# Optimization experiments

Measured on AMD Instinct MI355X. Metric: run time of the kernel, lower is better.

The kernel has to match this reference:

```python
import jax, jax.numpy as jnp
import numpy as np
from jax import lax

KH, KW = 9, 9
FC_DIM = 1024
C_RED = FC_DIM // 8  # 128
EPS = 1e-5


def conv_bn_relu(x, w, gamma, beta):
    # 3x3 conv, stride 1, pad 1 (NCHW / OIHW), then batch-stat BN + ReLU
    y = lax.conv_general_dilated(x, w, (1, 1), ((1, 1), (1, 1)),
                                 dimension_numbers=('NCHW', 'OIHW', 'NCHW'))
    mean = y.mean(axis=(0, 2, 3))
    var = y.var(axis=(0, 2, 3))
    y = (y - mean[None, :, None, None]) * lax.rsqrt(var + EPS)[None, :, None, None]
    y = y * gamma[None, :, None, None] + beta[None, :, None, None]
    return jnp.maximum(y, 0.0)


def local_weighting(feat, atten, kH, kW):
    # feat: [B,C,H,W]; atten: [B,H,W,kH*kW]
    # out[b,c,h,w] = sum_k atten[b,h,w,k] * feat_padded[b,c,h+dh_k,w+dw_k]
    B, C, H, W = feat.shape
    ph, pw = kH // 2, kW // 2
    fp = jnp.pad(feat, ((0, 0), (0, 0), (ph, ph), (pw, pw)))
    out = jnp.zeros_like(feat)
    k = 0
    for dh in range(kH):
        for dw in range(kW):
            out = out + fp[:, :, dh:dh + H, dw:dw + W] * atten[:, None, :, :, k]
            k += 1
    return out


def setup_inputs() -> dict:
    key = jax.random.key(0)
    ks = jax.random.split(key, 12)
    B, H, W = 4, 64, 64
    sc1 = 1.0 / np.sqrt(FC_DIM * 9)
    sc5 = 1.0 / np.sqrt(C_RED * 9)
    return {
        'low_key': jax.random.normal(ks[0], (B, FC_DIM, H, W), jnp.float32),
        'low_nonkey': jax.random.normal(ks[1], (B, FC_DIM, H, W), jnp.float32),
        'local_atten': jax.random.uniform(ks[2], (B, H, W, KH * KW), jnp.float32),
        'w1': jax.random.normal(ks[3], (C_RED, FC_DIM, 3, 3), jnp.float32) * sc1,
        'g1': jnp.ones((C_RED,), jnp.float32),
        'b1': jnp.zeros((C_RED,), jnp.float32),
        'w4': jax.random.normal(ks[4], (C_RED, FC_DIM, 3, 3), jnp.float32) * sc1,
        'g4': jnp.ones((C_RED,), jnp.float32),
        'b4': jnp.zeros((C_RED,), jnp.float32),
        'w5': jax.random.normal(ks[5], (C_RED, C_RED, 3, 3), jnp.float32) * sc5,
        'g5': jnp.ones((C_RED,), jnp.float32),
        'b5': jnp.zeros((C_RED,), jnp.float32),
        'fc1_w': jax.random.normal(ks[6], (10, C_RED), jnp.float32) * (1.0 / np.sqrt(C_RED)),
        'fc1_b': jnp.zeros((10,), jnp.float32),
        'fc2_w': jax.random.normal(ks[7], (1, 10), jnp.float32) * (1.0 / np.sqrt(10.0)),
        'fc2_b': jnp.zeros((1,), jnp.float32),
    }


def reference(low_key, low_nonkey, local_atten,
              w1, g1, b1, w4, g4, b4, w5, g5, b5,
              fc1_w, fc1_b, fc2_w, fc2_b):
    lk = conv_bn_relu(low_key, w1, g1, b1)          # [B,128,H,W]
    trans = local_weighting(lk, local_atten, KH, KW)
    lnk = conv_bn_relu(low_nonkey, w4, g4, b4)
    out = trans - lnk
    out = conv_bn_relu(out, w5, g5, b5)
    out = out.mean(axis=(2, 3))                      # adaptive avg pool to 1x1 -> [B,128]
    out = out @ fc1_w.T + fc1_b
    out = out @ fc2_w.T + fc2_b                      # [B,1]
    return out
```

## Files before the change

### kernel.cpp

```cpp
#include <hip/hip_runtime.h>
#include <hip/hip_bf16.h>


#define B_ 4
#define CM_ 128

typedef __attribute__((ext_vector_type(8))) short short8;
typedef __attribute__((ext_vector_type(4))) float floatx4;
typedef __attribute__((address_space(3))) unsigned lds_as;
typedef __attribute__((address_space(1))) const unsigned glb_as;

__device__ inline short f2bf(float f) {
  union { float f; unsigned u; } v; v.f = f;
  unsigned r = v.u + 0x7fff + ((v.u >> 16) & 1);
  return (short)(r >> 16);
}

__global__ void wprep_kernel(const float* __restrict__ w, short* __restrict__ wpk,
                             int cin) {
  int e = blockIdx.x * 256 + threadIdx.x;
  if (e >= cin * 9 * 128) return;
  int icb = e & 31;
  int oc = (e >> 5) & 127;
  int tap = (e >> 12) % 9;
  int kb = e / (32 * 128 * 9);
  wpk[e] = f2bf(w[((size_t)oc * cin + kb * 32 + icb) * 9 + tap]);
}

template <int KB>
__global__ void xprep_kernel(const float* __restrict__ x, short* __restrict__ xt) {
  int kb = blockIdx.x >> 4, rg = blockIdx.x & 15;
  int b = blockIdx.y;
  int row = rg * 4 + (threadIdx.x >> 6);
  int col = threadIdx.x & 63;
  const float* xs = x + (((size_t)b * (KB * 32) + kb * 32) * 64 + row) * 64 + col;
  short* xd = xt + ((((size_t)b * KB + kb) * 64 + row) * 64 + col) * 32;
  int sw = (col >> 1) & 3;
#pragma unroll
  for (int u = 0; u < 4; u++) {
    short8 pk;
#pragma unroll
    for (int j = 0; j < 8; j++) pk[j] = f2bf(xs[(size_t)(u * 8 + j) * 4096]);
    *(short8*)(xd + (u ^ sw) * 8) = pk;
  }
}

template <int KB>
__global__ __launch_bounds__(512, 2)
void convm_kernel(const short* __restrict__ xt, const short* __restrict__ wpk,
                  float* __restrict__ y) {
  __shared__ __attribute__((aligned(16))) short lx[16896];
  int tid = threadIdx.x;
  int lane = tid & 63;
  int wv = tid >> 6;
  int n16 = lane & 15, quad = lane >> 4;
  int pb = blockIdx.x;
  int b = pb >> 5, h0 = (pb & 31) * 2;
  int oc0 = blockIdx.y * 64 + (wv & 3) * 16;
  int ng = wv >> 2;

  if (tid < 256) {
    int reg = tid >> 4, dw = tid & 15;
    int bu = reg >> 3, rr = (reg >> 1) & 3, cl = reg & 1;
    *(int*)(lx + bu * 8448 + rr * 2112 + (cl ? 65 : 0) * 32 + dw * 2) = 0;
  }
  if (h0 == 0)
    for (int i = tid; i < 2112; i += 512) {
      int bu = i >= 1056; int o = i - bu * 1056;
      *((int*)lx + bu * 4224 + o) = 0;
    }
  if (h0 == 62)
    for (int i = tid; i < 2112; i += 512) {
      int bu = i >= 1056; int o = i - bu * 1056;
      *((int*)lx + bu * 4224 + 3 * 1056 + o) = 0;
    }

  auto dma = [&](int kb, int buf) {
#pragma unroll
    for (int t = 0; t < 2; t++) {
      int idx = wv * 2 + t;
      int r = idx >> 2, cc = idx & 3;
      int row = h0 - 1 + r;
      if (row >= 0 && row < 64) {
        const short* src = xt + ((((size_t)b * KB + kb) * 64 + row) * 64 + cc * 16) * 32 + lane * 8;
        short* dst = lx + buf * 8448 + r * 2112 + (1 + cc * 16) * 32 + lane * 8;
        __builtin_amdgcn_global_load_lds((glb_as*)src, (lds_as*)dst, 16, 0, 0);
      }
    }
  };

  const short* wb = wpk + (size_t)(oc0 + n16) * 32 + quad * 8;
  short8 afr[9], afn[9];
  dma(0, 0);
#pragma unroll
  for (int t = 0; t < 9; t++) afr[t] = *(const short8*)(wb + t * 4096);

  floatx4 acc[4];
#pragma unroll
  for (int nt = 0; nt < 4; nt++) acc[nt] = (floatx4){0.f, 0.f, 0.f, 0.f};

  for (int kb = 0; kb < KB; kb++) {
    __syncthreads();
    if (kb + 1 < KB) {
      dma(kb + 1, (kb + 1) & 1);
      const short* wn = wb + (size_t)(kb + 1) * 36864;
#pragma unroll
      for (int t = 0; t < 9; t++) afn[t] = *(const short8*)(wn + t * 4096);
    }
    const short* lb = lx + (kb & 1) * 8448;
#pragma unroll
    for (int tap = 0; tap < 9; tap++) {
      int r = tap / 3, s = tap % 3;
      const short* lr = lb + (ng + r) * 2112;
#pragma unroll
      for (int nt = 0; nt < 4; nt++) {
        int c = nt * 16 + n16 + s - 1;
        int uu = quad ^ ((c >> 1) & 3);
        short8 bf = *(const short8*)(lr + (c + 1) * 32 + uu * 8);
        acc[nt] = __builtin_amdgcn_mfma_f32_16x16x32_bf16(afr[tap], bf, acc[nt], 0, 0, 0);
      }
    }
    if (kb + 1 < KB) {
#pragma unroll
      for (int t = 0; t < 9; t++) afr[t] = afn[t];
    }
  }

  int row = h0 + ng, col = lane & 15;
#pragma unroll
  for (int nt = 0; nt < 4; nt++)
#pragma unroll
    for (int rg = 0; rg < 4; rg++) {
      int oc = oc0 + quad * 4 + rg;
      y[(((size_t)b * CM_ + oc) * 64 + row) * 64 + nt * 16 + col] = acc[nt][rg];
    }
}

__global__ void bnstats_kernel(const float* __restrict__ y, const float* __restrict__ g,
                               const float* __restrict__ bt, float2* __restrict__ scsh) {
  int c = blockIdx.x;
  int tid = threadIdx.x;
  float s = 0.f, s2 = 0.f;
  for (int b = 0; b < B_; b++) {
    const float4* p = (const float4*)(y + ((size_t)(b * CM_) + c) * 4096);
    for (int i = tid; i < 1024; i += 256) {
      float4 v = p[i];
      s += v.x + v.y + v.z + v.w;
      s2 += v.x * v.x + v.y * v.y + v.z * v.z + v.w * v.w;
    }
  }
  for (int off = 32; off > 0; off >>= 1) {
    s += __shfl_down(s, off);
    s2 += __shfl_down(s2, off);
  }
  __shared__ float rs[4], rq[4];
  if ((tid & 63) == 0) { rs[tid >> 6] = s; rq[tid >> 6] = s2; }
  __syncthreads();
  if (tid == 0) {
    float S = rs[0] + rs[1] + rs[2] + rs[3];
    float Q = rq[0] + rq[1] + rq[2] + rq[3];
    float mean = S * (1.f / 16384.f);
    float var = Q * (1.f / 16384.f) - mean * mean;
    float sc = g[c] * rsqrtf(var + 1e-5f);
    scsh[c] = make_float2(sc, bt[c] - mean * sc);
  }
}

__global__ __launch_bounds__(256, 2)
void localw_kernel(const float* __restrict__ y1, const float2* __restrict__ scsh1,
                   const float* __restrict__ y4, const float2* __restrict__ scsh4,
                   const float* __restrict__ atten, short* __restrict__ xt5) {
  __shared__ float at[81][65];
  __shared__ float lk[16][9][72];
  int bh = blockIdx.x;
  int b = bh >> 6, h = bh & 63;
  int c0 = blockIdx.y * 16;
  int tid = threadIdx.x;

  const float* ap = atten + ((size_t)b * 4096 + h * 64) * 81;
  for (int e = tid; e < 64 * 81; e += 256) {
    int w_ = e / 81, k = e % 81;
    at[k][w_] = ap[w_ * 81 + k];
  }
  for (int e = tid; e < 16 * 9 * 72; e += 256) {
    int c = e / (9 * 72);
    int rem = e % (9 * 72);
    int r = rem / 72;
    int j = rem % 72;
    int row = h + r - 4;
    int col = j - 4;
    float v = 0.f;
    if (row >= 0 && row < 64 && col >= 0 && col < 64) {
      float2 ss = scsh1[c0 + c];
      v = fmaxf(0.f, y1[((size_t)(b * CM_) + c0 + c) * 4096 + row * 64 + col] * ss.x + ss.y);
    }
    lk[c][r][j] = v;
  }
  __syncthreads();

  int lane = tid & 63;
  int wv = tid >> 6;
  float acc[4] = {0.f, 0.f, 0.f, 0.f};
  for (int r = 0; r < 9; r++) {
    float a[9];
#pragma unroll
    for (int dw = 0; dw < 9; dw++) a[dw] = at[r * 9 + dw][lane];
#pragma unroll
    for (int cc = 0; cc < 4; cc++) {
      int c = wv * 4 + cc;
#pragma unroll
      for (int dw = 0; dw < 9; dw++)
        acc[cc] = fmaf(a[dw], lk[c][r][lane + dw], acc[cc]);
    }
  }
#pragma unroll
  for (int cc = 0; cc < 4; cc++) {
    int c = c0 + wv * 4 + cc;
    float2 ss4 = scsh4[c];
    float lnk = fmaxf(0.f, y4[((size_t)(b * CM_) + c) * 4096 + h * 64 + lane] * ss4.x + ss4.y);
    float dv = acc[cc] - lnk;
    int icb = c & 31;
    int uu = (icb >> 3) ^ ((lane >> 1) & 3);
    xt5[((((size_t)b * 4 + (c >> 5)) * 64 + h) * 64 + lane) * 32 + uu * 8 + (icb & 7)] = f2bf(dv);
  }
}

__global__ void pool_kernel(const float* __restrict__ y, const float2* __restrict__ scsh,
                            float* __restrict__ pooled) {
  int bc = blockIdx.x;
  int c = bc & 127;
  float2 ss = scsh[c];
  const float4* p = (const float4*)(y + (size_t)bc * 4096);
  float s = 0.f;
  for (int i = threadIdx.x; i < 1024; i += 256) {
    float4 v = p[i];
    s += fmaxf(0.f, v.x * ss.x + ss.y) + fmaxf(0.f, v.y * ss.x + ss.y) +
         fmaxf(0.f, v.z * ss.x + ss.y) + fmaxf(0.f, v.w * ss.x + ss.y);
  }
  for (int off = 32; off > 0; off >>= 1) s += __shfl_down(s, off);
  __shared__ float rs[4];
  if ((threadIdx.x & 63) == 0) rs[threadIdx.x >> 6] = s;
  __syncthreads();
  if (threadIdx.x == 0) pooled[bc] = (rs[0] + rs[1] + rs[2] + rs[3]) * (1.f / 4096.f);
}

__global__ void fc_kernel(const float* __restrict__ pooled, const float* __restrict__ fc1w,
                          const float* __restrict__ fc1b, const float* __restrict__ fc2w,
                          const float* __restrict__ fc2b, float* __restrict__ out) {
  int lane = threadIdx.x;
  float p[B_][10];
#pragma unroll
  for (int b = 0; b < B_; b++)
#pragma unroll
    for (int j = 0; j < 10; j++) p[b][j] = 0.f;
  for (int c = lane; c < CM_; c += 64) {
#pragma unroll
    for (int b = 0; b < B_; b++) {
      float pv = pooled[b * CM_ + c];
#pragma unroll
      for (int j = 0; j < 10; j++) p[b][j] = fmaf(pv, fc1w[j * CM_ + c], p[b][j]);
    }
  }
  for (int off = 32; off > 0; off >>= 1)
#pragma unroll
    for (int b = 0; b < B_; b++)
#pragma unroll
      for (int j = 0; j < 10; j++) p[b][j] += __shfl_down(p[b][j], off);
  if (lane == 0) {
    for (int b = 0; b < B_; b++) {
      float o = fc2b[0];
      for (int j = 0; j < 10; j++) o += fc2w[j] * (p[b][j] + fc1b[j]);
      out[b] = o;
    }
  }
}

extern "C" void kernel_launch(void* const* d_in, const int* in_sizes, int n_in,
                              void* d_out, int out_size, void* d_ws, size_t ws_size,
                              hipStream_t stream) {
  const float* low_key    = (const float*)d_in[0];
  const float* low_nonkey = (const float*)d_in[1];
  const float* atten      = (const float*)d_in[2];
  const float* w1  = (const float*)d_in[3];
  const float* g1  = (const float*)d_in[4];
  const float* b1  = (const float*)d_in[5];
  const float* w4  = (const float*)d_in[6];
  const float* g4  = (const float*)d_in[7];
  const float* b4  = (const float*)d_in[8];
  const float* w5  = (const float*)d_in[9];
  const float* g5  = (const float*)d_in[10];
  const float* b5  = (const float*)d_in[11];
  const float* fc1w = (const float*)d_in[12];
  const float* fc1b = (const float*)d_in[13];
  const float* fc2w = (const float*)d_in[14];
  const float* fc2b = (const float*)d_in[15];

  char* w8 = (char*)d_ws;
  short* wpk = (short*)w8;
  short* xt  = (short*)(w8 + 2359296);
  short* xt5 = (short*)(w8 + 2359296 + 33554432);
  float* y1  = (float*)(w8 + 2359296 + 33554432 + 4194304);
  float* y4  = y1 + 2097152;
  float2* scsh1 = (float2*)(y4 + 2097152);
  float2* scsh4 = scsh1 + CM_;
  float2* scsh5 = scsh4 + CM_;
  float* pooled = (float*)(scsh5 + CM_);
  float* out = (float*)d_out;

  wprep_kernel<<<4608, 256, 0, stream>>>(w1, wpk, 1024);
  xprep_kernel<32><<<dim3(512, 4), 256, 0, stream>>>(low_key, xt);
  convm_kernel<32><<<dim3(128, 2), 512, 0, stream>>>(xt, wpk, y1);
  bnstats_kernel<<<128, 256, 0, stream>>>(y1, g1, b1, scsh1);

  wprep_kernel<<<4608, 256, 0, stream>>>(w4, wpk, 1024);
  xprep_kernel<32><<<dim3(512, 4), 256, 0, stream>>>(low_nonkey, xt);
  convm_kernel<32><<<dim3(128, 2), 512, 0, stream>>>(xt, wpk, y4);
  bnstats_kernel<<<128, 256, 0, stream>>>(y4, g4, b4, scsh4);

  localw_kernel<<<dim3(256, 8), 256, 0, stream>>>(y1, scsh1, y4, scsh4, atten, xt5);

  wprep_kernel<<<576, 256, 0, stream>>>(w5, wpk, 128);
  convm_kernel<4><<<dim3(128, 2), 512, 0, stream>>>(xt5, wpk, y1);
  bnstats_kernel<<<128, 256, 0, stream>>>(y1, g5, b5, scsh5);

  pool_kernel<<<512, 256, 0, stream>>>(y1, scsh5, pooled);
  fc_kernel<<<1, 64, 0, stream>>>(pooled, fc1w, fc1b, fc2w, fc2b, out);
}
```

Baseline: 447.9 us.

## Retile conv waves for B-fragment reuse and restructure local weighting over row blocks

The conv kernel gives each wave a 32-channel by 32-column tile so each LDS B fragment feeds two MFMAs, halving LDS reads per MFMA at the cost of doubled weight-fragment registers. The local weighting stage gains a transpose kernel for attention and now computes 8 output rows per block from a bf16 LDS tile, reusing each loaded window across rows instead of reloading a 9-row halo per row. This adds a launch, bf16 rounding of intermediate features, and fewer blocks.

```diff
diff --git a/kernel.cpp b/kernel.cpp
--- a/kernel.cpp
+++ b/kernel.cpp
@@ -14,6 +14,10 @@
   union { float f; unsigned u; } v; v.f = f;
   unsigned r = v.u + 0x7fff + ((v.u >> 16) & 1);
   return (short)(r >> 16);
+}
+__device__ inline float bf2f(unsigned short u) {
+  union { unsigned u; float f; } v; v.u = ((unsigned)u) << 16;
+  return v.f;
 }
 
 __global__ void wprep_kernel(const float* __restrict__ w, short* __restrict__ wpk,
@@ -56,8 +60,9 @@
   int n16 = lane & 15, quad = lane >> 4;
   int pb = blockIdx.x;
   int b = pb >> 5, h0 = (pb & 31) * 2;
-  int oc0 = blockIdx.y * 64 + (wv & 3) * 16;
-  int ng = wv >> 2;
+  int oc0 = blockIdx.y * 64 + (wv & 1) * 32;
+  int ng = (wv >> 1) & 1;
+  int ch = wv >> 2;
 
   if (tid < 256) {
     int reg = tid >> 4, dw = tid & 15;
@@ -89,23 +94,33 @@
     }
   };
 
-  const short* wb = wpk + (size_t)(oc0 + n16) * 32 + quad * 8;
-  short8 afr[9], afn[9];
+  const short* wb0 = wpk + (size_t)(oc0 + n16) * 32 + quad * 8;
+  const short* wb1 = wb0 + 512;
+  short8 afr[2][9], afn[2][9];
   dma(0, 0);
 #pragma unroll
-  for (int t = 0; t < 9; t++) afr[t] = *(const short8*)(wb + t * 4096);
-
-  floatx4 acc[4];
-#pragma unroll
-  for (int nt = 0; nt < 4; nt++) acc[nt] = (floatx4){0.f, 0.f, 0.f, 0.f};
+  for (int t = 0; t < 9; t++) {
+    afr[0][t] = *(const short8*)(wb0 + t * 4096);
+    afr[1][t] = *(const short8*)(wb1 + t * 4096);
+  }
+
+  floatx4 acc[2][2];
+#pragma unroll
+  for (int i = 0; i < 2; i++)
+#pragma unroll
+    for (int t2 = 0; t2 < 2; t2++) acc[i][t2] = (floatx4){0.f, 0.f, 0.f, 0.f};
 
   for (int kb = 0; kb < KB; kb++) {
     __syncthreads();
     if (kb + 1 < KB) {
       dma(kb + 1, (kb + 1) & 1);
-      const short* wn = wb + (size_t)(kb + 1) * 36864;
-#pragma unroll
-      for (int t = 0; t < 9; t++) afn[t] = *(const short8*)(wn + t * 4096);
+      const short* wn0 = wb0 + (size_t)(kb + 1) * 36864;
+      const short* wn1 = wb1 + (size_t)(kb + 1) * 36864;
+#pragma unroll
+      for (int t = 0; t < 9; t++) {
+        afn[0][t] = *(const short8*)(wn0 + t * 4096);
+        afn[1][t] = *(const short8*)(wn1 + t * 4096);
+      }
     }
     const short* lb = lx + (kb & 1) * 8448;
 #pragma unroll
@@ -113,27 +128,30 @@
       int r = tap / 3, s = tap % 3;
       const short* lr = lb + (ng + r) * 2112;
 #pragma unroll
-      for (int nt = 0; nt < 4; nt++) {
-        int c = nt * 16 + n16 + s - 1;
+      for (int t2 = 0; t2 < 2; t2++) {
+        int c = (ch * 2 + t2) * 16 + n16 + s - 1;
         int uu = quad ^ ((c >> 1) & 3);
         short8 bf = *(const short8*)(lr + (c + 1) * 32 + uu * 8);
-        acc[nt] = __builtin_amdgcn_mfma_f32_16x16x32_bf16(afr[tap], bf, acc[nt], 0, 0, 0);
+        acc[0][t2] = __builtin_amdgcn_mfma_f32_16x16x32_bf16(afr[0][tap], bf, acc[0][t2], 0, 0, 0);
+        acc[1][t2] = __builtin_amdgcn_mfma_f32_16x16x32_bf16(afr[1][tap], bf, acc[1][t2], 0, 0, 0);
       }
     }
     if (kb + 1 < KB) {
 #pragma unroll
-      for (int t = 0; t < 9; t++) afr[t] = afn[t];
-    }
-  }
-
-  int row = h0 + ng, col = lane & 15;
-#pragma unroll
-  for (int nt = 0; nt < 4; nt++)
-#pragma unroll
-    for (int rg = 0; rg < 4; rg++) {
-      int oc = oc0 + quad * 4 + rg;
-      y[(((size_t)b * CM_ + oc) * 64 + row) * 64 + nt * 16 + col] = acc[nt][rg];
-    }
+      for (int t = 0; t < 9; t++) { afr[0][t] = afn[0][t]; afr[1][t] = afn[1][t]; }
+    }
+  }
+
+  int row = h0 + ng, col = n16;
+#pragma unroll
+  for (int i = 0; i < 2; i++)
+#pragma unroll
+    for (int t2 = 0; t2 < 2; t2++)
+#pragma unroll
+      for (int rg = 0; rg < 4; rg++) {
+        int oc = oc0 + i * 16 + quad * 4 + rg;
+        y[(((size_t)b * CM_ + oc) * 64 + row) * 64 + (ch * 2 + t2) * 16 + col] = acc[i][t2][rg];
+      }
 }
 
 __global__ void bnstats_kernel(const float* __restrict__ y, const float* __restrict__ g,
@@ -166,62 +184,91 @@
   }
 }
 
-__global__ __launch_bounds__(256, 2)
+__global__ void attprep_kernel(const float* __restrict__ atten, float* __restrict__ att_t) {
+  __shared__ float tile[5184];
+  int b = blockIdx.x >> 6;
+  int p0 = (blockIdx.x & 63) * 64;
+  const float* src = atten + ((size_t)b * 4096 + p0) * 81;
+  for (int e = threadIdx.x; e < 5184; e += 256) tile[e] = src[e];
+  __syncthreads();
+  for (int f = threadIdx.x; f < 5184; f += 256) {
+    int k = f >> 6, w_ = f & 63;
+    att_t[((size_t)b * 81 + k) * 4096 + p0 + w_] = tile[w_ * 81 + k];
+  }
+}
+
+__global__ __launch_bounds__(256)
 void localw_kernel(const float* __restrict__ y1, const float2* __restrict__ scsh1,
                    const float* __restrict__ y4, const float2* __restrict__ scsh4,
-                   const float* __restrict__ atten, short* __restrict__ xt5) {
-  __shared__ float at[81][65];
-  __shared__ float lk[16][9][72];
-  int bh = blockIdx.x;
-  int b = bh >> 6, h = bh & 63;
-  int c0 = blockIdx.y * 16;
+                   const float* __restrict__ att_t, short* __restrict__ xt5) {
+  __shared__ unsigned short lkb[16][16][72];
+  int bx = blockIdx.x;
+  int b = bx >> 3, h0 = (bx & 7) * 8;
+  int cg = blockIdx.y;
   int tid = threadIdx.x;
-
-  const float* ap = atten + ((size_t)b * 4096 + h * 64) * 81;
-  for (int e = tid; e < 64 * 81; e += 256) {
-    int w_ = e / 81, k = e % 81;
-    at[k][w_] = ap[w_ * 81 + k];
-  }
-  for (int e = tid; e < 16 * 9 * 72; e += 256) {
-    int c = e / (9 * 72);
-    int rem = e % (9 * 72);
-    int r = rem / 72;
-    int j = rem % 72;
-    int row = h + r - 4;
-    int col = j - 4;
-    float v = 0.f;
-    if (row >= 0 && row < 64 && col >= 0 && col < 64) {
-      float2 ss = scsh1[c0 + c];
-      v = fmaxf(0.f, y1[((size_t)(b * CM_) + c0 + c) * 4096 + row * 64 + col] * ss.x + ss.y);
-    }
-    lk[c][r][j] = v;
-  }
-  __syncthreads();
-
   int lane = tid & 63;
   int wv = tid >> 6;
-  float acc[4] = {0.f, 0.f, 0.f, 0.f};
-  for (int r = 0; r < 9; r++) {
-    float a[9];
-#pragma unroll
-    for (int dw = 0; dw < 9; dw++) a[dw] = at[r * 9 + dw][lane];
-#pragma unroll
-    for (int cc = 0; cc < 4; cc++) {
-      int c = wv * 4 + cc;
-#pragma unroll
-      for (int dw = 0; dw < 9; dw++)
-        acc[cc] = fmaf(a[dw], lk[c][r][lane + dw], acc[cc]);
-    }
-  }
-#pragma unroll
-  for (int cc = 0; cc < 4; cc++) {
-    int c = c0 + wv * 4 + cc;
+
+  for (int c_l = 0; c_l < 16; c_l++) {
+    float2 ss = scsh1[cg * 16 + c_l];
+    const float* yp = y1 + ((size_t)(b * CM_) + cg * 16 + c_l) * 4096;
+    for (int e = tid; e < 16 * 72; e += 256) {
+      int gri = e / 72, j = e % 72;
+      int row = h0 - 4 + gri, col = j - 4;
+      float v = 0.f;
+      if (row >= 0 && row < 64 && col >= 0 && col < 64)
+        v = fmaxf(0.f, yp[row * 64 + col] * ss.x + ss.y);
+      lkb[c_l][gri][j] = (unsigned short)f2bf(v);
+    }
+  }
+  __syncthreads();
+
+  float acc[4][8];
+#pragma unroll
+  for (int cc = 0; cc < 4; cc++)
+#pragma unroll
+    for (int h_i = 0; h_i < 8; h_i++) acc[cc][h_i] = 0.f;
+
+  const float* ab = att_t + (size_t)b * 81 * 4096 + h0 * 64 + lane;
+
+  for (int gri = 0; gri < 16; ++gri) {
+    float win[4][9];
+#pragma unroll
+    for (int cc = 0; cc < 4; ++cc)
+#pragma unroll
+      for (int dw = 0; dw < 9; ++dw)
+        win[cc][dw] = bf2f(lkb[wv * 4 + cc][gri][lane + dw]);
+#pragma unroll
+    for (int h_i = 0; h_i < 8; ++h_i) {
+      int r = gri - h_i;
+      if (r < 0 || r > 8) continue;
+      const float* ap = ab + (size_t)(r * 9) * 4096 + h_i * 64;
+      float a[9];
+#pragma unroll
+      for (int dw = 0; dw < 9; ++dw) a[dw] = ap[(size_t)dw * 4096];
+#pragma unroll
+      for (int cc = 0; cc < 4; ++cc)
+#pragma unroll
+        for (int dw = 0; dw < 9; ++dw)
+          acc[cc][h_i] = fmaf(a[dw], win[cc][dw], acc[cc][h_i]);
+    }
+  }
+
+#pragma unroll
+  for (int cc = 0; cc < 4; ++cc) {
+    int c = cg * 16 + wv * 4 + cc;
     float2 ss4 = scsh4[c];
-    float lnk = fmaxf(0.f, y4[((size_t)(b * CM_) + c) * 4096 + h * 64 + lane] * ss4.x + ss4.y);
-    float dv = acc[cc] - lnk;
     int icb = c & 31;
     int uu = (icb >> 3) ^ ((lane >> 1) & 3);
-    xt5[((((size_t)b * 4 + (c >> 5)) * 64 + h) * 64 + lane) * 32 + uu * 8 + (icb & 7)] = f2bf(dv);
+#pragma unroll
+    for (int h_i = 0; h_i < 8; ++h_i) {
+      int h = h0 + h_i;
+      size_t gi = ((size_t)(b * CM_) + c) * 4096 + h * 64 + lane;
+      float lnk = fmaxf(0.f, y4[gi] * ss4.x + ss4.y);
+      float dv = acc[cc][h_i] - lnk;
+      xt5[((((size_t)b * 4 + (c >> 5)) * 64 + h) * 64 + lane) * 32 + uu * 8 + (icb & 7)] =
+          f2bf(dv);
+    }
   }
 }
 
@@ -305,6 +352,7 @@
   float2* scsh4 = scsh1 + CM_;
   float2* scsh5 = scsh4 + CM_;
   float* pooled = (float*)(scsh5 + CM_);
+  float* att_t = (float*)xt;
   float* out = (float*)d_out;
 
   wprep_kernel<<<4608, 256, 0, stream>>>(w1, wpk, 1024);
@@ -317,7 +365,9 @@
   convm_kernel<32><<<dim3(128, 2), 512, 0, stream>>>(xt, wpk, y4);
   bnstats_kernel<<<128, 256, 0, stream>>>(y4, g4, b4, scsh4);
 
-  localw_kernel<<<dim3(256, 8), 256, 0, stream>>>(y1, scsh1, y4, scsh4, atten, xt5);
+  attprep_kernel<<<256, 256, 0, stream>>>(atten, att_t);
+
+  localw_kernel<<<dim3(32, 8), 256, 0, stream>>>(y1, scsh1, y4, scsh4, att_t, xt5);
 
   wprep_kernel<<<576, 256, 0, stream>>>(w5, wpk, 128);
   convm_kernel<4><<<dim3(128, 2), 512, 0, stream>>>(xt5, wpk, y1);
```

Result: slower. 508.1 us (+13.4%).
